# Kernel tuning notes

Measured on AMD Instinct MI355X. Metric: run time of the kernel, lower is better.

Reference implementation:

```python
import jax, jax.numpy as jnp
import numpy as np

E = 8192
K = 16
P = E * K
HIDDEN = 128
HEADS = 8
HEAD_DIM = HIDDEN // HEADS  # 16
NRAD = 64
CUTOFF = 10.0
EPS = 1e-5


def _rbf(d):
    # Gaussian radial basis expansion on [0, cutoff]
    centers = jnp.linspace(0.0, CUTOFF, NRAD)
    width = CUTOFF / NRAD
    return jnp.exp(-(((d[..., None] - centers) / width) ** 2))  # [..., NRAD]


def setup_inputs() -> dict:
    key = jax.random.key(0)
    ks = jax.random.split(key, 24)

    def lin_w(k, fi, fo):
        s = 1.0 / np.sqrt(fi)
        return jax.random.uniform(k, (fi, fo), minval=-s, maxval=s, dtype=jnp.float32)

    def lin_b(k, fi, fo):
        s = 1.0 / np.sqrt(fi)
        return jax.random.uniform(k, (fo,), minval=-s, maxval=s, dtype=jnp.float32)

    edge_features = jax.random.normal(ks[0], (E, HIDDEN), dtype=jnp.float32)
    edge_coords = jax.random.normal(ks[1], (E, 3), dtype=jnp.float32) * 3.0
    # K neighbors per edge: row index repeated, neighbor index random
    src = jnp.repeat(jnp.arange(E, dtype=jnp.int32), K)
    dst = jax.random.randint(ks[2], (P,), 0, E, dtype=jnp.int32)
    edge_pairs = jnp.stack([src, dst], axis=-1)  # [P, 2]

    mlp_in = HEAD_DIM * 2 + NRAD + 1  # 97
    return {
        "edge_features": edge_features,
        "edge_coords": edge_coords,
        "Wq": lin_w(ks[3], HIDDEN, HIDDEN),
        "Wk": lin_w(ks[4], HIDDEN, HIDDEN),
        "Wv": lin_w(ks[5], HIDDEN, HIDDEN),
        "W1": lin_w(ks[6], mlp_in, HIDDEN), "b1": lin_b(ks[7], mlp_in, HIDDEN),
        "W2": lin_w(ks[8], HIDDEN, HIDDEN), "b2": lin_b(ks[9], HIDDEN, HIDDEN),
        "W3": lin_w(ks[10], HIDDEN, HEADS), "b3": lin_b(ks[11], HIDDEN, HEADS),
        "Wg1": lin_w(ks[12], HEAD_DIM, HIDDEN), "bg1": lin_b(ks[13], HEAD_DIM, HIDDEN),
        "Wg2": lin_w(ks[14], HIDDEN, 1), "bg2": lin_b(ks[15], HIDDEN, 1),
        "Wo": lin_w(ks[16], HIDDEN, HIDDEN), "bo": lin_b(ks[17], HIDDEN, HIDDEN),
        "gamma": jnp.ones((HIDDEN,), jnp.float32),
        "beta": jnp.zeros((HIDDEN,), jnp.float32),
        "edge_pairs": edge_pairs,
    }


def reference(edge_features, edge_coords, Wq, Wk, Wv, W1, b1, W2, b2, W3, b3,
              Wg1, bg1, Wg2, bg2, Wo, bo, gamma, beta, edge_pairs):
    E_ = edge_features.shape[0]
    src = edge_pairs[:, 0]
    dst = edge_pairs[:, 1]
    silu = jax.nn.silu

    q = (edge_features @ Wq).reshape(E_, HEADS, HEAD_DIM)
    k = (edge_features @ Wk).reshape(E_, HEADS, HEAD_DIM)
    v = (edge_features @ Wv).reshape(E_, HEADS, HEAD_DIM)

    coord_diff = edge_coords[src] - edge_coords[dst]        # [P, 3]
    dist = jnp.sqrt(jnp.sum(coord_diff * coord_diff, -1))   # [P]
    rb = _rbf(dist)                                         # [P, NRAD]

    feats = []
    coords = edge_coords
    for h in range(HEADS):  # fixed small loop over structurally distinct heads
        qp = q[src, h]                                      # [P, HEAD_DIM]
        kp = k[dst, h]
        vp = v[dst, h]
        dot = jnp.sum(qp * kp, -1, keepdims=True)           # [P, 1]
        x = jnp.concatenate([qp, kp, rb, dot], axis=-1)     # [P, 97]
        hmid = silu(silu(x @ W1 + b1) @ W2 + b2)            # [P, HIDDEN]
        scores = (hmid @ W3 + b3)[:, h]                     # [P]
        # scatter softmax over destination rows (src index)
        m = jax.ops.segment_max(scores, src, num_segments=E_)
        w = jnp.exp(scores - m[src])
        denom = jax.ops.segment_sum(w, src, num_segments=E_)
        attn = w / denom[src]                               # [P]
        agg = jax.ops.segment_sum(attn[:, None] * vp, src, num_segments=E_)
        feats.append(agg)
        # equivariant coordinate update
        gate = jax.nn.sigmoid(silu(vp @ Wg1 + bg1) @ Wg2 + bg2)  # [P, 1]
        cu = jax.ops.segment_sum(attn[:, None] * gate * coord_diff, src,
                                 num_segments=E_)
        coords = coords + cu / HEADS

    uf = jnp.concatenate(feats, axis=-1)                    # [E, HIDDEN]
    y = edge_features + uf @ Wo + bo
    mean = jnp.mean(y, -1, keepdims=True)
    var = jnp.mean((y - mean) ** 2, -1, keepdims=True)
    yn = (y - mean) / jnp.sqrt(var + EPS) * gamma + beta
    return yn, coords
```

## Files before the change

kernel.cpp:

```cpp
#include <hip/hip_runtime.h>
#include <hip/hip_bf16.h>
#include <math.h>

#define E_N   8192
#define K_N   16
#define HID   128
#define HEADS 8
#define HD    16
#define NRAD  64

typedef unsigned short ushort_t;
typedef __attribute__((ext_vector_type(8))) short bf16x8;
typedef __attribute__((ext_vector_type(4))) float f32x4;
typedef __attribute__((ext_vector_type(2))) float f32x2;

__device__ __forceinline__ float fast_rcp(float x){ return __builtin_amdgcn_rcpf(x); }
__device__ __forceinline__ float silu_f(float x){ return x * fast_rcp(1.f + __expf(-x)); }
__device__ __forceinline__ float sigmoid_f(float x){ return fast_rcp(1.f + __expf(-x)); }

__device__ __forceinline__ ushort_t f2b(float x){
  union { __hip_bfloat16 b; ushort_t u; } cv;
  cv.b = __float2bfloat16(x);
  return cv.u;
}
__device__ __forceinline__ unsigned int pk_bf16(float a, float b){
  unsigned int r;
  asm volatile("v_cvt_pk_bf16_f32 %0, %1, %2" : "=v"(r) : "v"(a), "v"(b));
  return r;
}

__device__ __forceinline__ unsigned int silu2(f32x2 x){
  f32x2 t;
  t.x = __expf(-x.x);
  t.y = __expf(-x.y);
  f32x2 d = t + 1.f;
  f32x2 r;
  r.x = fast_rcp(d.x);
  r.y = fast_rcp(d.y);
  f32x2 y = x * r;
  return pk_bf16(y.x, y.y);
}

__device__ __forceinline__ void* lds_h(ushort_t* base, int row, int col){
  unsigned int byte = ((unsigned int)(row*256 + col*2)) ^ (((unsigned int)(row & 7)) << 4);
  return (void*)(reinterpret_cast<char*>(base) + byte);
}

__global__ __launch_bounds__(256) void wprep_kernel(
    const float* __restrict__ W1, const float* __restrict__ W2, const float* __restrict__ W3,
    const float* __restrict__ b1,
    const float* __restrict__ Wq, const float* __restrict__ Wk, const float* __restrict__ Wv,
    ushort_t* __restrict__ W1f, ushort_t* __restrict__ W2f, ushort_t* __restrict__ W3f,
    ushort_t* __restrict__ Wqf, ushort_t* __restrict__ Wkf, ushort_t* __restrict__ Wvf)
{
  int idx = blockIdx.x*256 + threadIdx.x;
  if (idx < 32768){
    int id  = idx & 16383;
    int i  = id & 7;
    int l  = (id >> 3) & 63;
    int nf = (id >> 9) & 7;
    int ks = (id >> 12) & 3;
    int kk = ks*32 + (l>>4)*8 + i;
    int n  = (nf>>1)*32 + 2*(l&15) + (nf&1);
    if (idx < 16384){
      float val = (kk < 97) ? W1[kk*128 + n] : (kk == 97 ? b1[n] : 0.f);
      W1f[id] = f2b(val);
    } else {
      W2f[id] = f2b(W2[kk*128 + n]);
    }
  } else if (idx < 34816){
    int id = idx - 32768;
    int i  = id & 7;
    int l  = (id >> 3) & 63;
    int ks = (id >> 9) & 3;
    int kk = ks*32 + (l>>4)*8 + i;
    int n  = l & 15;
    W3f[id] = (n < 8) ? f2b(W3[kk*8 + n]) : (ushort_t)0;
  } else if (idx < 83968){
    int id = idx - 34816;
    int m  = id >> 14;
    int r  = id & 16383;
    int i  = r & 7;
    int l  = (r >> 3) & 63;
    int nf = (r >> 9) & 7;
    int ks = (r >> 12) & 3;
    int kk = ks*32 + (l>>4)*8 + i;
    int n  = nf*16 + (l&15);
    const float* Wm = (m==0) ? Wq : ((m==1) ? Wk : Wv);
    ushort_t*    Dm = (m==0) ? Wqf : ((m==1) ? Wkf : Wvf);
    Dm[r] = f2b(Wm[kk*128 + n]);
  }
}

__global__ __launch_bounds__(256) void qkv_mfma(
    const float* __restrict__ ef,
    const ushort_t* __restrict__ Wqf, const ushort_t* __restrict__ Wkf,
    const ushort_t* __restrict__ Wvf,
    float* __restrict__ q, float* __restrict__ k, float* __restrict__ v)
{
  __shared__ __align__(16) ushort_t EfT[64*128];
  const int t = threadIdx.x;
  const int w  = t >> 6;
  const int l  = t & 63;
  const int lr = l & 15;
  const int lg = l >> 4;
  const int base = blockIdx.x * 64;

  {
    int r = t >> 2, qr = t & 3;
    const float4* src = reinterpret_cast<const float4*>(ef + (base + r)*128 + qr*32);
    #pragma unroll
    for (int i4=0;i4<8;i4++){
      float4 xv = src[i4];
      *reinterpret_cast<unsigned int*>(lds_h(EfT, r, qr*32 + i4*4    )) = pk_bf16(xv.x, xv.y);
      *reinterpret_cast<unsigned int*>(lds_h(EfT, r, qr*32 + i4*4 + 2)) = pk_bf16(xv.z, xv.w);
    }
  }
  __syncthreads();

  bf16x8 Afr[4][4];
  #pragma unroll
  for (int mf=0;mf<4;mf++)
    #pragma unroll
    for (int ks=0;ks<4;ks++)
      Afr[mf][ks] = *reinterpret_cast<const bf16x8*>(lds_h(EfT, mf*16 + lr, ks*32 + lg*8));

  #pragma unroll
  for (int m=0;m<3;m++){
    const ushort_t* Wf = (m==0) ? Wqf : ((m==1) ? Wkf : Wvf);
    float*          Om = (m==0) ? q   : ((m==1) ? k   : v);
    f32x4 acc[4][2];
    #pragma unroll
    for (int mf=0;mf<4;mf++){ acc[mf][0] = (f32x4)0.f; acc[mf][1] = (f32x4)0.f; }
    #pragma unroll
    for (int ks=0; ks<4; ks++){
      bf16x8 B0 = *reinterpret_cast<const bf16x8*>(Wf + ((ks*8 + w*2+0)*64 + l)*8);
      bf16x8 B1 = *reinterpret_cast<const bf16x8*>(Wf + ((ks*8 + w*2+1)*64 + l)*8);
      #pragma unroll
      for (int mf=0; mf<4; mf++){
        acc[mf][0] = __builtin_amdgcn_mfma_f32_16x16x32_bf16(Afr[mf][ks], B0, acc[mf][0], 0,0,0);
        acc[mf][1] = __builtin_amdgcn_mfma_f32_16x16x32_bf16(Afr[mf][ks], B1, acc[mf][1], 0,0,0);
      }
    }
    #pragma unroll
    for (int mf=0;mf<4;mf++)
      #pragma unroll
      for (int nf=0;nf<2;nf++)
        #pragma unroll
        for (int i=0;i<4;i++){
          int row = base + mf*16 + lg*4 + i;
          int col = w*32 + nf*16 + lr;
          Om[row*128 + col] = acc[mf][nf][i];
        }
  }
}

__global__ __launch_bounds__(256) void gate_kernel(
    const float* __restrict__ v,
    const float* __restrict__ Wg1, const float* __restrict__ bg1,
    const float* __restrict__ Wg2, const float* __restrict__ bg2,
    float* __restrict__ gate)
{
  const int e = blockIdx.x;
  const int t = threadIdx.x;
  const int h = t >> 5, l = t & 31;
  float vp[16];
  #pragma unroll
  for (int i=0;i<16;i++) vp[i] = v[e*128 + h*16 + i];
  float part = 0.f;
  #pragma unroll
  for (int jj=0;jj<4;jj++){
    int j = l + jj*32;
    float a = bg1[j];
    #pragma unroll
    for (int i=0;i<16;i++) a += vp[i]*Wg1[i*128+j];
    part += silu_f(a) * Wg2[j];
  }
  #pragma unroll
  for (int off=16; off>=1; off>>=1) part += __shfl_xor(part, off, 64);
  if (l==0) gate[e*8+h] = sigmoid_f(part + bg2[0]);
}

__global__ __launch_bounds__(256) void edge_attn_mfma(
    const float* __restrict__ ef, const float* __restrict__ coords,
    const float* __restrict__ q, const float* __restrict__ k, const float* __restrict__ v,
    const ushort_t* __restrict__ W1f, const ushort_t* __restrict__ W2f,
    const ushort_t* __restrict__ W3f,
    const float* __restrict__ b2, const float* __restrict__ b3,
    const float* __restrict__ Wo, const float* __restrict__ bo,
    const float* __restrict__ gamma, const float* __restrict__ beta,
    const int* __restrict__ pairs, const float* __restrict__ gate,
    float* __restrict__ out_y, float* __restrict__ out_c)
{
  __shared__ __align__(16) ushort_t BufA[128*128];
  __shared__ __align__(16) float SmallBuf[416];
  __shared__ float cd_l[16][4];
  __shared__ float gate_l[16][8];
  __shared__ int   dstl[16];

  float* sc_l   = SmallBuf;
  float* attn_l = SmallBuf + 128;
  float* feats  = SmallBuf + 256;
  float* red    = SmallBuf + 384;
  float* wopart = SmallBuf;

  const int e = blockIdx.x;
  const int t = threadIdx.x;
  const int w  = t >> 6;
  const int l  = t & 63;
  const int lr = l & 15;
  const int lg = l >> 4;

  const int pg   = lg;
  const int p    = w*4 + pg;
  const int dstp = pairs[(e*16 + p)*2 + 1];
  if (l < 4) dstl[w*4 + l] = pairs[(e*16 + w*4 + l)*2 + 1];

  float cx = coords[e*3+0]-coords[dstp*3+0];
  float cy = coords[e*3+1]-coords[dstp*3+1];
  float cz = coords[e*3+2]-coords[dstp*3+2];
  float dist = sqrtf(cx*cx+cy*cy+cz*cz);
  if (lr < 3) cd_l[p][lr] = (lr==0) ? cx : (lr==1 ? cy : cz);

  {
    int i0 = lr * 4;
    float z0 = (dist - (float)(i0+0)*(10.0f/63.0f)) * 6.4f;
    float z1 = (dist - (float)(i0+1)*(10.0f/63.0f)) * 6.4f;
    float z2 = (dist - (float)(i0+2)*(10.0f/63.0f)) * 6.4f;
    float z3 = (dist - (float)(i0+3)*(10.0f/63.0f)) * 6.4f;
    unsigned int u01 = pk_bf16(__expf(-z0*z0), __expf(-z1*z1));
    unsigned int u23 = pk_bf16(__expf(-z2*z2), __expf(-z3*z3));
    int base_row = w*32 + pg*8;
    #pragma unroll
    for (int rr=0; rr<8; rr++){
      *reinterpret_cast<unsigned int*>(lds_h(BufA, base_row+rr, 32+i0  )) = u01;
      *reinterpret_cast<unsigned int*>(lds_h(BufA, base_row+rr, 32+i0+2)) = u23;
    }
  }

  {
    const int rl  = l >> 1;
    const int hf  = l & 1;
    const int row = w*32 + rl;
    const int hh  = rl & 7;
    float dot = 0.f;
    if (hf == 0){
      const float4* qp4 = reinterpret_cast<const float4*>(q + e*128 + hh*16);
      const float4* kp4 = reinterpret_cast<const float4*>(k + dstp*128 + hh*16);
      #pragma unroll
      for (int i4=0;i4<4;i4++){
        float4 qv = qp4[i4], kv = kp4[i4];
        dot += qv.x*kv.x + qv.y*kv.y + qv.z*kv.z + qv.w*kv.w;
        *reinterpret_cast<unsigned int*>(lds_h(BufA, row, i4*4     )) = pk_bf16(qv.x, qv.y);
        *reinterpret_cast<unsigned int*>(lds_h(BufA, row, i4*4+2   )) = pk_bf16(qv.z, qv.w);
        *reinterpret_cast<unsigned int*>(lds_h(BufA, row, 16+i4*4  )) = pk_bf16(kv.x, kv.y);
        *reinterpret_cast<unsigned int*>(lds_h(BufA, row, 16+i4*4+2)) = pk_bf16(kv.z, kv.w);
      }
    }
    float dsw = __shfl_xor(dot, 1, 64);
    if (hf == 1){
      *reinterpret_cast<unsigned int*>(lds_h(BufA, row, 96)) = pk_bf16(dsw, 1.0f);
      #pragma unroll
      for (int c=98;c<128;c+=2)
        *reinterpret_cast<unsigned int*>(lds_h(BufA, row, c)) = 0u;
    }
  }
  __syncthreads();

  const int c0 = w*32 + 2*lr;
  const f32x2 b2p = { b2[c0], b2[c0+1] };

  #pragma unroll
  for (int pass=0; pass<2; ++pass){
    f32x4 acc[4][2];
    #pragma unroll
    for (int mf=0;mf<4;mf++){ acc[mf][0] = (f32x4)0.f; acc[mf][1] = (f32x4)0.f; }
    #pragma unroll
    for (int ks=0; ks<4; ks++){
      bf16x8 B0 = *reinterpret_cast<const bf16x8*>(W1f + ((ks*8 + w*2+0)*64 + l)*8);
      bf16x8 B1 = *reinterpret_cast<const bf16x8*>(W1f + ((ks*8 + w*2+1)*64 + l)*8);
      #pragma unroll
      for (int mf=0; mf<4; mf++){
        bf16x8 A = *reinterpret_cast<const bf16x8*>(lds_h(BufA, pass*64 + mf*16 + lr, ks*32 + lg*8));
        acc[mf][0] = __builtin_amdgcn_mfma_f32_16x16x32_bf16(A, B0, acc[mf][0], 0,0,0);
        acc[mf][1] = __builtin_amdgcn_mfma_f32_16x16x32_bf16(A, B1, acc[mf][1], 0,0,0);
      }
    }
    __syncthreads();
    #pragma unroll
    for (int mf=0;mf<4;mf++){
      #pragma unroll
      for (int i=0;i<4;i++){
        int row = pass*64 + mf*16 + lg*4 + i;
        f32x2 x2 = { acc[mf][0][i], acc[mf][1][i] };
        *reinterpret_cast<unsigned int*>(lds_h(BufA, row, c0)) = silu2(x2);
      }
    }
  }

  #pragma unroll
  for (int pass=0; pass<2; ++pass){
    f32x4 acc[4][2];
    #pragma unroll
    for (int mf=0;mf<4;mf++){ acc[mf][0] = (f32x4)0.f; acc[mf][1] = (f32x4)0.f; }
    #pragma unroll
    for (int ks=0; ks<4; ks++){
      bf16x8 B0 = *reinterpret_cast<const bf16x8*>(W2f + ((ks*8 + w*2+0)*64 + l)*8);
      bf16x8 B1 = *reinterpret_cast<const bf16x8*>(W2f + ((ks*8 + w*2+1)*64 + l)*8);
      #pragma unroll
      for (int mf=0; mf<4; mf++){
        bf16x8 A = *reinterpret_cast<const bf16x8*>(lds_h(BufA, pass*64 + mf*16 + lr, ks*32 + lg*8));
        acc[mf][0] = __builtin_amdgcn_mfma_f32_16x16x32_bf16(A, B0, acc[mf][0], 0,0,0);
        acc[mf][1] = __builtin_amdgcn_mfma_f32_16x16x32_bf16(A, B1, acc[mf][1], 0,0,0);
      }
    }
    __syncthreads();
    #pragma unroll
    for (int mf=0;mf<4;mf++){
      #pragma unroll
      for (int i=0;i<4;i++){
        int row = pass*64 + mf*16 + lg*4 + i;
        f32x2 x2 = (f32x2){ acc[mf][0][i], acc[mf][1][i] } + b2p;
        *reinterpret_cast<unsigned int*>(lds_h(BufA, row, c0)) = silu2(x2);
      }
    }
  }
  __syncthreads();

  {
    f32x4 a0 = (f32x4)0.f, a1 = (f32x4)0.f;
    #pragma unroll
    for (int ks=0; ks<4; ks++){
      bf16x8 B3 = *reinterpret_cast<const bf16x8*>(W3f + (ks*64 + l)*8);
      bf16x8 A0 = *reinterpret_cast<const bf16x8*>(lds_h(BufA, (w*2+0)*16 + lr, ks*32 + lg*8));
      bf16x8 A1 = *reinterpret_cast<const bf16x8*>(lds_h(BufA, (w*2+1)*16 + lr, ks*32 + lg*8));
      a0 = __builtin_amdgcn_mfma_f32_16x16x32_bf16(A0, B3, a0, 0,0,0);
      a1 = __builtin_amdgcn_mfma_f32_16x16x32_bf16(A1, B3, a1, 0,0,0);
    }
    #pragma unroll
    for (int i=0;i<4;i++){
      int rin = lg*4 + i;
      if (lr == (rin & 7)){
        sc_l[(w*2+0)*16 + rin] = a0[i] + b3[rin & 7];
        sc_l[(w*2+1)*16 + rin] = a1[i] + b3[rin & 7];
      }
    }
  }
  __syncthreads();

  if (t < 8){
    const int h = t;
    float m = -1e30f;
    for (int pp=0;pp<16;pp++) m = fmaxf(m, sc_l[pp*8+h]);
    float den = 0.f;
    for (int pp=0;pp<16;pp++){ float wgt = __expf(sc_l[pp*8+h]-m); attn_l[pp*8+h]=wgt; den += wgt; }
    float inv = fast_rcp(den);
    for (int pp=0;pp<16;pp++) attn_l[pp*8+h] *= inv;
  }
  if (t >= 128){
    int idx = t - 128; int pp = idx>>3, h = idx&7;
    gate_l[pp][h] = gate[dstl[pp]*8 + h];
  }
  __syncthreads();

  if (t < 128){
    const int h = t >> 4;
    float s = 0.f;
    #pragma unroll
    for (int pp=0;pp<16;pp++) s += attn_l[pp*8+h] * v[dstl[pp]*128 + t];
    feats[t] = s;
  }
  if (t >= 128 && t < 144){
    int pp = t-128;
    float s = 0.f;
    #pragma unroll
    for (int h=0;h<8;h++) s += attn_l[pp*8+h]*gate_l[pp][h];
    cd_l[pp][3] = s;
  }
  __syncthreads();
  if (t < 3){
    float s = 0.f;
    #pragma unroll
    for (int pp=0;pp<16;pp++) s += cd_l[pp][3]*cd_l[pp][t];
    out_c[e*3+t] = coords[e*3+t] + s*0.125f;
  }

  {
    const int col  = t & 127;
    const int half = t >> 7;
    f32x2 a2 = {0.f, 0.f};
    const float* feats2 = feats + half*64;
    const float* Wocol  = Wo + half*64*128 + col;
    #pragma unroll
    for (int iq=0; iq<32; iq++){
      f32x2 x2 = *reinterpret_cast<const f32x2*>(feats2 + iq*2);
      f32x2 w2 = { Wocol[(iq*2)*128], Wocol[(iq*2+1)*128] };
      a2 += x2 * w2;
    }
    __syncthreads();
    wopart[t] = a2.x + a2.y;
  }
  __syncthreads();

  float yv = 0.f;
  if (t < 128){
    yv = ef[e*128+t] + wopart[t] + wopart[t+128] + bo[t];
    float s1 = yv, s2 = yv*yv;
    #pragma unroll
    for (int off=32; off>=1; off>>=1){ s1 += __shfl_xor(s1,off,64); s2 += __shfl_xor(s2,off,64); }
    if ((t&63)==0){ red[(t>>6)*2+0]=s1; red[(t>>6)*2+1]=s2; }
  }
  __syncthreads();
  if (t < 128){
    float sm = red[0]+red[2], sq = red[1]+red[3];
    float mean = sm * (1.f/128.f);
    float var  = sq * (1.f/128.f) - mean*mean;
    float rstd = rsqrtf(var + 1e-5f);
    out_y[e*128+t] = (yv-mean)*rstd*gamma[t] + beta[t];
  }
}

extern "C" void kernel_launch(void* const* d_in, const int* in_sizes, int n_in,
                              void* d_out, int out_size, void* d_ws, size_t ws_size,
                              hipStream_t stream)
{
  const float* ef     = (const float*)d_in[0];
  const float* coords = (const float*)d_in[1];
  const float* Wq  = (const float*)d_in[2];
  const float* Wk  = (const float*)d_in[3];
  const float* Wv  = (const float*)d_in[4];
  const float* W1  = (const float*)d_in[5];
  const float* b1  = (const float*)d_in[6];
  const float* W2  = (const float*)d_in[7];
  const float* b2  = (const float*)d_in[8];
  const float* W3  = (const float*)d_in[9];
  const float* b3  = (const float*)d_in[10];
  const float* Wg1 = (const float*)d_in[11];
  const float* bg1 = (const float*)d_in[12];
  const float* Wg2 = (const float*)d_in[13];
  const float* bg2 = (const float*)d_in[14];
  const float* Wo  = (const float*)d_in[15];
  const float* bo  = (const float*)d_in[16];
  const float* gamma = (const float*)d_in[17];
  const float* beta  = (const float*)d_in[18];
  const int*   pairs = (const int*)d_in[19];

  float* ws   = (float*)d_ws;
  float* q    = ws;
  float* k    = q + E_N*HID;
  float* v    = k + E_N*HID;
  float* gate = v + E_N*HID;
  ushort_t* W1f = (ushort_t*)(gate + E_N*HEADS);
  ushort_t* W2f = W1f + 16384;
  ushort_t* W3f = W2f + 16384;
  ushort_t* Wqf = W3f + 2048;
  ushort_t* Wkf = Wqf + 16384;
  ushort_t* Wvf = Wkf + 16384;

  wprep_kernel<<<328, 256, 0, stream>>>(W1, W2, W3, b1, Wq, Wk, Wv,
      W1f, W2f, W3f, Wqf, Wkf, Wvf);
  qkv_mfma<<<E_N/64, 256, 0, stream>>>(ef, Wqf, Wkf, Wvf, q, k, v);
  gate_kernel<<<E_N, 256, 0, stream>>>(v, Wg1, bg1, Wg2, bg2, gate);
  edge_attn_mfma<<<E_N, 256, 0, stream>>>(ef, coords, q, k, v,
      W1f, W2f, W3f, b2, b3, Wo, bo, gamma, beta, pairs, gate,
      (float*)d_out, (float*)d_out + E_N*HID);
}
```

Baseline: 195.3 us.

## Split edge MLP rows across eight waves instead of two-pass loop

Launches the edge attention kernel with 512 threads so the 128-row MLP tile is split across eight waves (two row halves by four column slices), removing the two-pass loop per layer. The score projection now uses one 16-row tile per wave. Setup, Wo projection and reductions are limited to the first 256 threads. This raises per-block parallelism but leaves half the threads idle in several stages, adds barriers, and may reduce the number of resident blocks per CU.

```diff
diff --git a/kernel.cpp b/kernel.cpp
--- a/kernel.cpp
+++ b/kernel.cpp
@@ -181,7 +181,7 @@
   if (l==0) gate[e*8+h] = sigmoid_f(part + bg2[0]);
 }
 
-__global__ __launch_bounds__(256) void edge_attn_mfma(
+__global__ __launch_bounds__(512) void edge_attn_mfma(
     const float* __restrict__ ef, const float* __restrict__ coords,
     const float* __restrict__ q, const float* __restrict__ k, const float* __restrict__ v,
     const ushort_t* __restrict__ W1f, const ushort_t* __restrict__ W2f,
@@ -211,139 +211,134 @@
   const int lr = l & 15;
   const int lg = l >> 4;
 
-  const int pg   = lg;
-  const int p    = w*4 + pg;
-  const int dstp = pairs[(e*16 + p)*2 + 1];
-  if (l < 4) dstl[w*4 + l] = pairs[(e*16 + w*4 + l)*2 + 1];
-
-  float cx = coords[e*3+0]-coords[dstp*3+0];
-  float cy = coords[e*3+1]-coords[dstp*3+1];
-  float cz = coords[e*3+2]-coords[dstp*3+2];
-  float dist = sqrtf(cx*cx+cy*cy+cz*cz);
-  if (lr < 3) cd_l[p][lr] = (lr==0) ? cx : (lr==1 ? cy : cz);
+  if (t < 256){
+    const int pg   = lg;
+    const int p    = w*4 + pg;
+    const int dstp = pairs[(e*16 + p)*2 + 1];
+    if (l < 4) dstl[w*4 + l] = pairs[(e*16 + w*4 + l)*2 + 1];
+
+    float cx = coords[e*3+0]-coords[dstp*3+0];
+    float cy = coords[e*3+1]-coords[dstp*3+1];
+    float cz = coords[e*3+2]-coords[dstp*3+2];
+    float dist = sqrtf(cx*cx+cy*cy+cz*cz);
+    if (lr < 3) cd_l[p][lr] = (lr==0) ? cx : (lr==1 ? cy : cz);
+
+    {
+      int i0 = lr * 4;
+      float z0 = (dist - (float)(i0+0)*(10.0f/63.0f)) * 6.4f;
+      float z1 = (dist - (float)(i0+1)*(10.0f/63.0f)) * 6.4f;
+      float z2 = (dist - (float)(i0+2)*(10.0f/63.0f)) * 6.4f;
+      float z3 = (dist - (float)(i0+3)*(10.0f/63.0f)) * 6.4f;
+      unsigned int u01 = pk_bf16(__expf(-z0*z0), __expf(-z1*z1));
+      unsigned int u23 = pk_bf16(__expf(-z2*z2), __expf(-z3*z3));
+      int base_row = w*32 + pg*8;
+      #pragma unroll
+      for (int rr=0; rr<8; rr++){
+        *reinterpret_cast<unsigned int*>(lds_h(BufA, base_row+rr, 32+i0  )) = u01;
+        *reinterpret_cast<unsigned int*>(lds_h(BufA, base_row+rr, 32+i0+2)) = u23;
+      }
+    }
+
+    {
+      const int rl  = l >> 1;
+      const int hf  = l & 1;
+      const int row = w*32 + rl;
+      const int hh  = rl & 7;
+      float dot = 0.f;
+      if (hf == 0){
+        const float4* qp4 = reinterpret_cast<const float4*>(q + e*128 + hh*16);
+        const float4* kp4 = reinterpret_cast<const float4*>(k + dstp*128 + hh*16);
+        #pragma unroll
+        for (int i4=0;i4<4;i4++){
+          float4 qv = qp4[i4], kv = kp4[i4];
+          dot += qv.x*kv.x + qv.y*kv.y + qv.z*kv.z + qv.w*kv.w;
+          *reinterpret_cast<unsigned int*>(lds_h(BufA, row, i4*4     )) = pk_bf16(qv.x, qv.y);
+          *reinterpret_cast<unsigned int*>(lds_h(BufA, row, i4*4+2   )) = pk_bf16(qv.z, qv.w);
+          *reinterpret_cast<unsigned int*>(lds_h(BufA, row, 16+i4*4  )) = pk_bf16(kv.x, kv.y);
+          *reinterpret_cast<unsigned int*>(lds_h(BufA, row, 16+i4*4+2)) = pk_bf16(kv.z, kv.w);
+        }
+      }
+      float dsw = __shfl_xor(dot, 1, 64);
+      if (hf == 1){
+        *reinterpret_cast<unsigned int*>(lds_h(BufA, row, 96)) = pk_bf16(dsw, 1.0f);
+        #pragma unroll
+        for (int c=98;c<128;c+=2)
+          *reinterpret_cast<unsigned int*>(lds_h(BufA, row, c)) = 0u;
+      }
+    }
+  }
+  __syncthreads();
+
+  const int wm = w >> 2;
+  const int wn = w & 3;
+  const int c0 = wn*32 + 2*lr;
+  const f32x2 b2p = { b2[c0], b2[c0+1] };
+
+  f32x4 acc[4][2];
+
+  #pragma unroll
+  for (int mf=0;mf<4;mf++){ acc[mf][0] = (f32x4)0.f; acc[mf][1] = (f32x4)0.f; }
+  #pragma unroll
+  for (int ks=0; ks<4; ks++){
+    bf16x8 B0 = *reinterpret_cast<const bf16x8*>(W1f + ((ks*8 + wn*2+0)*64 + l)*8);
+    bf16x8 B1 = *reinterpret_cast<const bf16x8*>(W1f + ((ks*8 + wn*2+1)*64 + l)*8);
+    #pragma unroll
+    for (int mf=0; mf<4; mf++){
+      bf16x8 A = *reinterpret_cast<const bf16x8*>(lds_h(BufA, wm*64 + mf*16 + lr, ks*32 + lg*8));
+      acc[mf][0] = __builtin_amdgcn_mfma_f32_16x16x32_bf16(A, B0, acc[mf][0], 0,0,0);
+      acc[mf][1] = __builtin_amdgcn_mfma_f32_16x16x32_bf16(A, B1, acc[mf][1], 0,0,0);
+    }
+  }
+  __syncthreads();
+  #pragma unroll
+  for (int mf=0;mf<4;mf++){
+    #pragma unroll
+    for (int i=0;i<4;i++){
+      int row = wm*64 + mf*16 + lg*4 + i;
+      f32x2 x2 = { acc[mf][0][i], acc[mf][1][i] };
+      *reinterpret_cast<unsigned int*>(lds_h(BufA, row, c0)) = silu2(x2);
+    }
+  }
+  __syncthreads();
+
+  #pragma unroll
+  for (int mf=0;mf<4;mf++){ acc[mf][0] = (f32x4)0.f; acc[mf][1] = (f32x4)0.f; }
+  #pragma unroll
+  for (int ks=0; ks<4; ks++){
+    bf16x8 B0 = *reinterpret_cast<const bf16x8*>(W2f + ((ks*8 + wn*2+0)*64 + l)*8);
+    bf16x8 B1 = *reinterpret_cast<const bf16x8*>(W2f + ((ks*8 + wn*2+1)*64 + l)*8);
+    #pragma unroll
+    for (int mf=0; mf<4; mf++){
+      bf16x8 A = *reinterpret_cast<const bf16x8*>(lds_h(BufA, wm*64 + mf*16 + lr, ks*32 + lg*8));
+      acc[mf][0] = __builtin_amdgcn_mfma_f32_16x16x32_bf16(A, B0, acc[mf][0], 0,0,0);
+      acc[mf][1] = __builtin_amdgcn_mfma_f32_16x16x32_bf16(A, B1, acc[mf][1], 0,0,0);
+    }
+  }
+  __syncthreads();
+  #pragma unroll
+  for (int mf=0;mf<4;mf++){
+    #pragma unroll
+    for (int i=0;i<4;i++){
+      int row = wm*64 + mf*16 + lg*4 + i;
+      f32x2 x2 = (f32x2){ acc[mf][0][i], acc[mf][1][i] } + b2p;
+      *reinterpret_cast<unsigned int*>(lds_h(BufA, row, c0)) = silu2(x2);
+    }
+  }
+  __syncthreads();
 
   {
-    int i0 = lr * 4;
-    float z0 = (dist - (float)(i0+0)*(10.0f/63.0f)) * 6.4f;
-    float z1 = (dist - (float)(i0+1)*(10.0f/63.0f)) * 6.4f;
-    float z2 = (dist - (float)(i0+2)*(10.0f/63.0f)) * 6.4f;
-    float z3 = (dist - (float)(i0+3)*(10.0f/63.0f)) * 6.4f;
-    unsigned int u01 = pk_bf16(__expf(-z0*z0), __expf(-z1*z1));
-    unsigned int u23 = pk_bf16(__expf(-z2*z2), __expf(-z3*z3));
-    int base_row = w*32 + pg*8;
-    #pragma unroll
-    for (int rr=0; rr<8; rr++){
-      *reinterpret_cast<unsigned int*>(lds_h(BufA, base_row+rr, 32+i0  )) = u01;
-      *reinterpret_cast<unsigned int*>(lds_h(BufA, base_row+rr, 32+i0+2)) = u23;
-    }
-  }
-
-  {
-    const int rl  = l >> 1;
-    const int hf  = l & 1;
-    const int row = w*32 + rl;
-    const int hh  = rl & 7;
-    float dot = 0.f;
-    if (hf == 0){
-      const float4* qp4 = reinterpret_cast<const float4*>(q + e*128 + hh*16);
-      const float4* kp4 = reinterpret_cast<const float4*>(k + dstp*128 + hh*16);
-      #pragma unroll
-      for (int i4=0;i4<4;i4++){
-        float4 qv = qp4[i4], kv = kp4[i4];
-        dot += qv.x*kv.x + qv.y*kv.y + qv.z*kv.z + qv.w*kv.w;
-        *reinterpret_cast<unsigned int*>(lds_h(BufA, row, i4*4     )) = pk_bf16(qv.x, qv.y);
-        *reinterpret_cast<unsigned int*>(lds_h(BufA, row, i4*4+2   )) = pk_bf16(qv.z, qv.w);
-        *reinterpret_cast<unsigned int*>(lds_h(BufA, row, 16+i4*4  )) = pk_bf16(kv.x, kv.y);
-        *reinterpret_cast<unsigned int*>(lds_h(BufA, row, 16+i4*4+2)) = pk_bf16(kv.z, kv.w);
-      }
-    }
-    float dsw = __shfl_xor(dot, 1, 64);
-    if (hf == 1){
-      *reinterpret_cast<unsigned int*>(lds_h(BufA, row, 96)) = pk_bf16(dsw, 1.0f);
-      #pragma unroll
-      for (int c=98;c<128;c+=2)
-        *reinterpret_cast<unsigned int*>(lds_h(BufA, row, c)) = 0u;
-    }
-  }
-  __syncthreads();
-
-  const int c0 = w*32 + 2*lr;
-  const f32x2 b2p = { b2[c0], b2[c0+1] };
-
-  #pragma unroll
-  for (int pass=0; pass<2; ++pass){
-    f32x4 acc[4][2];
-    #pragma unroll
-    for (int mf=0;mf<4;mf++){ acc[mf][0] = (f32x4)0.f; acc[mf][1] = (f32x4)0.f; }
-    #pragma unroll
-    for (int ks=0; ks<4; ks++){
-      bf16x8 B0 = *reinterpret_cast<const bf16x8*>(W1f + ((ks*8 + w*2+0)*64 + l)*8);
-      bf16x8 B1 = *reinterpret_cast<const bf16x8*>(W1f + ((ks*8 + w*2+1)*64 + l)*8);
-      #pragma unroll
-      for (int mf=0; mf<4; mf++){
-        bf16x8 A = *reinterpret_cast<const bf16x8*>(lds_h(BufA, pass*64 + mf*16 + lr, ks*32 + lg*8));
-        acc[mf][0] = __builtin_amdgcn_mfma_f32_16x16x32_bf16(A, B0, acc[mf][0], 0,0,0);
-        acc[mf][1] = __builtin_amdgcn_mfma_f32_16x16x32_bf16(A, B1, acc[mf][1], 0,0,0);
-      }
-    }
-    __syncthreads();
-    #pragma unroll
-    for (int mf=0;mf<4;mf++){
-      #pragma unroll
-      for (int i=0;i<4;i++){
-        int row = pass*64 + mf*16 + lg*4 + i;
-        f32x2 x2 = { acc[mf][0][i], acc[mf][1][i] };
-        *reinterpret_cast<unsigned int*>(lds_h(BufA, row, c0)) = silu2(x2);
-      }
-    }
-  }
-
-  #pragma unroll
-  for (int pass=0; pass<2; ++pass){
-    f32x4 acc[4][2];
-    #pragma unroll
-    for (int mf=0;mf<4;mf++){ acc[mf][0] = (f32x4)0.f; acc[mf][1] = (f32x4)0.f; }
-    #pragma unroll
-    for (int ks=0; ks<4; ks++){
-      bf16x8 B0 = *reinterpret_cast<const bf16x8*>(W2f + ((ks*8 + w*2+0)*64 + l)*8);
-      bf16x8 B1 = *reinterpret_cast<const bf16x8*>(W2f + ((ks*8 + w*2+1)*64 + l)*8);
-      #pragma unroll
-      for (int mf=0; mf<4; mf++){
-        bf16x8 A = *reinterpret_cast<const bf16x8*>(lds_h(BufA, pass*64 + mf*16 + lr, ks*32 + lg*8));
-        acc[mf][0] = __builtin_amdgcn_mfma_f32_16x16x32_bf16(A, B0, acc[mf][0], 0,0,0);
-        acc[mf][1] = __builtin_amdgcn_mfma_f32_16x16x32_bf16(A, B1, acc[mf][1], 0,0,0);
-      }
-    }
-    __syncthreads();
-    #pragma unroll
-    for (int mf=0;mf<4;mf++){
-      #pragma unroll
-      for (int i=0;i<4;i++){
-        int row = pass*64 + mf*16 + lg*4 + i;
-        f32x2 x2 = (f32x2){ acc[mf][0][i], acc[mf][1][i] } + b2p;
-        *reinterpret_cast<unsigned int*>(lds_h(BufA, row, c0)) = silu2(x2);
-      }
-    }
-  }
-  __syncthreads();
-
-  {
-    f32x4 a0 = (f32x4)0.f, a1 = (f32x4)0.f;
+    f32x4 a0 = (f32x4)0.f;
     #pragma unroll
     for (int ks=0; ks<4; ks++){
       bf16x8 B3 = *reinterpret_cast<const bf16x8*>(W3f + (ks*64 + l)*8);
-      bf16x8 A0 = *reinterpret_cast<const bf16x8*>(lds_h(BufA, (w*2+0)*16 + lr, ks*32 + lg*8));
-      bf16x8 A1 = *reinterpret_cast<const bf16x8*>(lds_h(BufA, (w*2+1)*16 + lr, ks*32 + lg*8));
+      bf16x8 A0 = *reinterpret_cast<const bf16x8*>(lds_h(BufA, w*16 + lr, ks*32 + lg*8));
       a0 = __builtin_amdgcn_mfma_f32_16x16x32_bf16(A0, B3, a0, 0,0,0);
-      a1 = __builtin_amdgcn_mfma_f32_16x16x32_bf16(A1, B3, a1, 0,0,0);
     }
     #pragma unroll
     for (int i=0;i<4;i++){
       int rin = lg*4 + i;
-      if (lr == (rin & 7)){
-        sc_l[(w*2+0)*16 + rin] = a0[i] + b3[rin & 7];
-        sc_l[(w*2+1)*16 + rin] = a1[i] + b3[rin & 7];
-      }
+      if (lr == (rin & 7))
+        sc_l[w*16 + rin] = a0[i] + b3[rin & 7];
     }
   }
   __syncthreads();
@@ -357,7 +352,7 @@
     float inv = fast_rcp(den);
     for (int pp=0;pp<16;pp++) attn_l[pp*8+h] *= inv;
   }
-  if (t >= 128){
+  if (t >= 128 && t < 256){
     int idx = t - 128; int pp = idx>>3, h = idx&7;
     gate_l[pp][h] = gate[dstl[pp]*8 + h];
   }
@@ -385,10 +380,10 @@
     out_c[e*3+t] = coords[e*3+t] + s*0.125f;
   }
 
-  {
+  f32x2 a2 = {0.f, 0.f};
+  if (t < 256){
     const int col  = t & 127;
     const int half = t >> 7;
-    f32x2 a2 = {0.f, 0.f};
     const float* feats2 = feats + half*64;
     const float* Wocol  = Wo + half*64*128 + col;
     #pragma unroll
@@ -397,9 +392,9 @@
       f32x2 w2 = { Wocol[(iq*2)*128], Wocol[(iq*2+1)*128] };
       a2 += x2 * w2;
     }
-    __syncthreads();
-    wopart[t] = a2.x + a2.y;
-  }
+  }
+  __syncthreads();
+  if (t < 256) wopart[t] = a2.x + a2.y;
   __syncthreads();
 
   float yv = 0.f;
@@ -461,7 +456,7 @@
       W1f, W2f, W3f, Wqf, Wkf, Wvf);
   qkv_mfma<<<E_N/64, 256, 0, stream>>>(ef, Wqf, Wkf, Wvf, q, k, v);
   gate_kernel<<<E_N, 256, 0, stream>>>(v, Wg1, bg1, Wg2, bg2, gate);
-  edge_attn_mfma<<<E_N, 256, 0, stream>>>(ef, coords, q, k, v,
+  edge_attn_mfma<<<E_N, 512, 0, stream>>>(ef, coords, q, k, v,
       W1f, W2f, W3f, b2, b3, Wo, bo, gamma, beta, pairs, gate,
       (float*)d_out, (float*)d_out + E_N*HID);
 }
```

Result: slower. 216.0 us (+10.6%).

## Chain edge MLP layers in registers via transposed MFMA instead of LDS round-trips

Applied to the files above, without the earlier changes.

The three-layer edge MLP now runs in transposed form: each wave keeps its 32 rows of input in registers, computes W1^T·X with the weight as the A operand, and feeds the SiLU-packed bf16 accumulators directly as B operands to 16x16x16 MFMAs for W2 and W3. This removes the intermediate LDS writes, reads and __syncthreads between layers, and the weight prep kernel emits new transposed fragment layouts to match. In exchange it holds more live registers, which could lower occupancy, and it uses the smaller-K MFMA shape for the second and third layers.

```diff
diff --git a/kernel.cpp b/kernel.cpp
--- a/kernel.cpp
+++ b/kernel.cpp
@@ -11,6 +11,7 @@
 
 typedef unsigned short ushort_t;
 typedef __attribute__((ext_vector_type(8))) short bf16x8;
+typedef __attribute__((ext_vector_type(4))) short bf16x4;
 typedef __attribute__((ext_vector_type(4))) float f32x4;
 typedef __attribute__((ext_vector_type(2))) float f32x2;
 
@@ -40,6 +41,21 @@
   f32x2 y = x * r;
   return pk_bf16(y.x, y.y);
 }
+__device__ __forceinline__ bf16x4 silu_pack4(f32x4 x){
+  union { unsigned int u[2]; bf16x4 v; } cv;
+  cv.u[0] = silu2((f32x2){x[0], x[1]});
+  cv.u[1] = silu2((f32x2){x[2], x[3]});
+  return cv.v;
+}
+
+__device__ __forceinline__ f32x4 mfma16(bf16x4 a, bf16x4 b, f32x4 c){
+#if __has_builtin(__builtin_amdgcn_mfma_f32_16x16x16bf16_1k)
+  return __builtin_amdgcn_mfma_f32_16x16x16bf16_1k(a, b, c, 0, 0, 0);
+#else
+  asm volatile("v_mfma_f32_16x16x16_bf16 %0, %1, %2, %0" : "+v"(c) : "v"(a), "v"(b));
+  return c;
+#endif
+}
 
 __device__ __forceinline__ void* lds_h(ushort_t* base, int row, int col){
   unsigned int byte = ((unsigned int)(row*256 + col*2)) ^ (((unsigned int)(row & 7)) << 4);
@@ -50,32 +66,36 @@
     const float* __restrict__ W1, const float* __restrict__ W2, const float* __restrict__ W3,
     const float* __restrict__ b1,
     const float* __restrict__ Wq, const float* __restrict__ Wk, const float* __restrict__ Wv,
-    ushort_t* __restrict__ W1f, ushort_t* __restrict__ W2f, ushort_t* __restrict__ W3f,
+    ushort_t* __restrict__ W1t, ushort_t* __restrict__ W2t, ushort_t* __restrict__ W3t,
     ushort_t* __restrict__ Wqf, ushort_t* __restrict__ Wkf, ushort_t* __restrict__ Wvf)
 {
   int idx = blockIdx.x*256 + threadIdx.x;
-  if (idx < 32768){
-    int id  = idx & 16383;
-    int i  = id & 7;
-    int l  = (id >> 3) & 63;
-    int nf = (id >> 9) & 7;
-    int ks = (id >> 12) & 3;
+  if (idx < 16384){
+    int i  = idx & 7;
+    int l  = (idx >> 3) & 63;
+    int ks = (idx >> 9) & 3;
+    int ff = (idx >> 11) & 7;
     int kk = ks*32 + (l>>4)*8 + i;
-    int n  = (nf>>1)*32 + 2*(l&15) + (nf&1);
-    if (idx < 16384){
-      float val = (kk < 97) ? W1[kk*128 + n] : (kk == 97 ? b1[n] : 0.f);
-      W1f[id] = f2b(val);
-    } else {
-      W2f[id] = f2b(W2[kk*128 + n]);
-    }
+    int f  = ff*16 + (l&15);
+    float val = (kk < 97) ? W1[kk*128 + f] : (kk == 97 ? b1[f] : 0.f);
+    W1t[idx] = f2b(val);
+  } else if (idx < 32768){
+    int id = idx - 16384;
+    int i  = id & 3;
+    int l  = (id >> 2) & 63;
+    int ks = (id >> 8) & 7;
+    int gf = (id >> 11) & 7;
+    int f  = ks*16 + (l>>4)*4 + i;
+    int g  = gf*16 + (l&15);
+    W2t[id] = f2b(W2[f*128 + g]);
   } else if (idx < 34816){
     int id = idx - 32768;
-    int i  = id & 7;
-    int l  = (id >> 3) & 63;
-    int ks = (id >> 9) & 3;
-    int kk = ks*32 + (l>>4)*8 + i;
+    int i  = id & 3;
+    int l  = (id >> 2) & 63;
+    int ks = (id >> 8) & 7;
+    int g  = ks*16 + (l>>4)*4 + i;
     int n  = l & 15;
-    W3f[id] = (n < 8) ? f2b(W3[kk*8 + n]) : (ushort_t)0;
+    W3t[id] = (n < 8) ? f2b(W3[g*8 + n]) : (ushort_t)0;
   } else if (idx < 83968){
     int id = idx - 34816;
     int m  = id >> 14;
@@ -184,8 +204,8 @@
 __global__ __launch_bounds__(256) void edge_attn_mfma(
     const float* __restrict__ ef, const float* __restrict__ coords,
     const float* __restrict__ q, const float* __restrict__ k, const float* __restrict__ v,
-    const ushort_t* __restrict__ W1f, const ushort_t* __restrict__ W2f,
-    const ushort_t* __restrict__ W3f,
+    const ushort_t* __restrict__ W1t, const ushort_t* __restrict__ W2t,
+    const ushort_t* __restrict__ W3t,
     const float* __restrict__ b2, const float* __restrict__ b3,
     const float* __restrict__ Wo, const float* __restrict__ bo,
     const float* __restrict__ gamma, const float* __restrict__ beta,
@@ -267,84 +287,53 @@
   }
   __syncthreads();
 
-  const int c0 = w*32 + 2*lr;
-  const f32x2 b2p = { b2[c0], b2[c0+1] };
-
-  #pragma unroll
-  for (int pass=0; pass<2; ++pass){
-    f32x4 acc[4][2];
-    #pragma unroll
-    for (int mf=0;mf<4;mf++){ acc[mf][0] = (f32x4)0.f; acc[mf][1] = (f32x4)0.f; }
+  bf16x8 Xb[2][4];
+  #pragma unroll
+  for (int rf=0; rf<2; rf++)
+    #pragma unroll
+    for (int ks=0; ks<4; ks++)
+      Xb[rf][ks] = *reinterpret_cast<const bf16x8*>(
+          lds_h(BufA, w*32 + rf*16 + lr, ks*32 + lg*8));
+
+  bf16x4 B1s[8][2];
+  #pragma unroll
+  for (int ff=0; ff<8; ff++){
+    f32x4 a0 = (f32x4)0.f, a1 = (f32x4)0.f;
     #pragma unroll
     for (int ks=0; ks<4; ks++){
-      bf16x8 B0 = *reinterpret_cast<const bf16x8*>(W1f + ((ks*8 + w*2+0)*64 + l)*8);
-      bf16x8 B1 = *reinterpret_cast<const bf16x8*>(W1f + ((ks*8 + w*2+1)*64 + l)*8);
-      #pragma unroll
-      for (int mf=0; mf<4; mf++){
-        bf16x8 A = *reinterpret_cast<const bf16x8*>(lds_h(BufA, pass*64 + mf*16 + lr, ks*32 + lg*8));
-        acc[mf][0] = __builtin_amdgcn_mfma_f32_16x16x32_bf16(A, B0, acc[mf][0], 0,0,0);
-        acc[mf][1] = __builtin_amdgcn_mfma_f32_16x16x32_bf16(A, B1, acc[mf][1], 0,0,0);
-      }
-    }
-    __syncthreads();
-    #pragma unroll
-    for (int mf=0;mf<4;mf++){
-      #pragma unroll
-      for (int i=0;i<4;i++){
-        int row = pass*64 + mf*16 + lg*4 + i;
-        f32x2 x2 = { acc[mf][0][i], acc[mf][1][i] };
-        *reinterpret_cast<unsigned int*>(lds_h(BufA, row, c0)) = silu2(x2);
-      }
-    }
-  }
-
-  #pragma unroll
-  for (int pass=0; pass<2; ++pass){
-    f32x4 acc[4][2];
-    #pragma unroll
-    for (int mf=0;mf<4;mf++){ acc[mf][0] = (f32x4)0.f; acc[mf][1] = (f32x4)0.f; }
-    #pragma unroll
-    for (int ks=0; ks<4; ks++){
-      bf16x8 B0 = *reinterpret_cast<const bf16x8*>(W2f + ((ks*8 + w*2+0)*64 + l)*8);
-      bf16x8 B1 = *reinterpret_cast<const bf16x8*>(W2f + ((ks*8 + w*2+1)*64 + l)*8);
-      #pragma unroll
-      for (int mf=0; mf<4; mf++){
-        bf16x8 A = *reinterpret_cast<const bf16x8*>(lds_h(BufA, pass*64 + mf*16 + lr, ks*32 + lg*8));
-        acc[mf][0] = __builtin_amdgcn_mfma_f32_16x16x32_bf16(A, B0, acc[mf][0], 0,0,0);
-        acc[mf][1] = __builtin_amdgcn_mfma_f32_16x16x32_bf16(A, B1, acc[mf][1], 0,0,0);
-      }
-    }
-    __syncthreads();
-    #pragma unroll
-    for (int mf=0;mf<4;mf++){
-      #pragma unroll
-      for (int i=0;i<4;i++){
-        int row = pass*64 + mf*16 + lg*4 + i;
-        f32x2 x2 = (f32x2){ acc[mf][0][i], acc[mf][1][i] } + b2p;
-        *reinterpret_cast<unsigned int*>(lds_h(BufA, row, c0)) = silu2(x2);
-      }
-    }
-  }
-  __syncthreads();
-
-  {
-    f32x4 a0 = (f32x4)0.f, a1 = (f32x4)0.f;
-    #pragma unroll
-    for (int ks=0; ks<4; ks++){
-      bf16x8 B3 = *reinterpret_cast<const bf16x8*>(W3f + (ks*64 + l)*8);
-      bf16x8 A0 = *reinterpret_cast<const bf16x8*>(lds_h(BufA, (w*2+0)*16 + lr, ks*32 + lg*8));
-      bf16x8 A1 = *reinterpret_cast<const bf16x8*>(lds_h(BufA, (w*2+1)*16 + lr, ks*32 + lg*8));
-      a0 = __builtin_amdgcn_mfma_f32_16x16x32_bf16(A0, B3, a0, 0,0,0);
-      a1 = __builtin_amdgcn_mfma_f32_16x16x32_bf16(A1, B3, a1, 0,0,0);
-    }
-    #pragma unroll
-    for (int i=0;i<4;i++){
-      int rin = lg*4 + i;
-      if (lr == (rin & 7)){
-        sc_l[(w*2+0)*16 + rin] = a0[i] + b3[rin & 7];
-        sc_l[(w*2+1)*16 + rin] = a1[i] + b3[rin & 7];
-      }
-    }
+      bf16x8 A = *reinterpret_cast<const bf16x8*>(W1t + (ff*2048 + ks*512 + l*8));
+      a0 = __builtin_amdgcn_mfma_f32_16x16x32_bf16(A, Xb[0][ks], a0, 0,0,0);
+      a1 = __builtin_amdgcn_mfma_f32_16x16x32_bf16(A, Xb[1][ks], a1, 0,0,0);
+    }
+    B1s[ff][0] = silu_pack4(a0);
+    B1s[ff][1] = silu_pack4(a1);
+  }
+
+  f32x4 s0 = (f32x4)0.f, s1 = (f32x4)0.f;
+  #pragma unroll
+  for (int gf=0; gf<8; gf++){
+    f32x4 c0 = (f32x4)0.f, c1 = (f32x4)0.f;
+    #pragma unroll
+    for (int ks=0; ks<8; ks++){
+      bf16x4 A2 = *reinterpret_cast<const bf16x4*>(W2t + (gf*2048 + ks*256 + l*4));
+      c0 = mfma16(A2, B1s[ks][0], c0);
+      c1 = mfma16(A2, B1s[ks][1], c1);
+    }
+    f32x4 b2v = *reinterpret_cast<const f32x4*>(b2 + gf*16 + lg*4);
+    c0 += b2v;
+    c1 += b2v;
+    bf16x4 h0 = silu_pack4(c0);
+    bf16x4 h1 = silu_pack4(c1);
+    bf16x4 A3 = *reinterpret_cast<const bf16x4*>(W3t + (gf*256 + l*4));
+    s0 = mfma16(A3, h0, s0);
+    s1 = mfma16(A3, h1, s1);
+  }
+
+  if (lg == ((l & 7) >> 2)){
+    int i = l & 3;
+    float b3v = b3[l & 7];
+    sc_l[w*32 +      lr] = s0[i] + b3v;
+    sc_l[w*32 + 16 + lr] = s1[i] + b3v;
   }
   __syncthreads();
 
@@ -405,10 +394,10 @@
   float yv = 0.f;
   if (t < 128){
     yv = ef[e*128+t] + wopart[t] + wopart[t+128] + bo[t];
-    float s1 = yv, s2 = yv*yv;
-    #pragma unroll
-    for (int off=32; off>=1; off>>=1){ s1 += __shfl_xor(s1,off,64); s2 += __shfl_xor(s2,off,64); }
-    if ((t&63)==0){ red[(t>>6)*2+0]=s1; red[(t>>6)*2+1]=s2; }
+    float s1v = yv, s2v = yv*yv;
+    #pragma unroll
+    for (int off=32; off>=1; off>>=1){ s1v += __shfl_xor(s1v,off,64); s2v += __shfl_xor(s2v,off,64); }
+    if ((t&63)==0){ red[(t>>6)*2+0]=s1v; red[(t>>6)*2+1]=s2v; }
   }
   __syncthreads();
   if (t < 128){
@@ -450,18 +439,18 @@
   float* k    = q + E_N*HID;
   float* v    = k + E_N*HID;
   float* gate = v + E_N*HID;
-  ushort_t* W1f = (ushort_t*)(gate + E_N*HEADS);
-  ushort_t* W2f = W1f + 16384;
-  ushort_t* W3f = W2f + 16384;
-  ushort_t* Wqf = W3f + 2048;
+  ushort_t* W1t = (ushort_t*)(gate + E_N*HEADS);
+  ushort_t* W2t = W1t + 16384;
+  ushort_t* W3t = W2t + 16384;
+  ushort_t* Wqf = W3t + 2048;
   ushort_t* Wkf = Wqf + 16384;
   ushort_t* Wvf = Wkf + 16384;
 
   wprep_kernel<<<328, 256, 0, stream>>>(W1, W2, W3, b1, Wq, Wk, Wv,
-      W1f, W2f, W3f, Wqf, Wkf, Wvf);
+      W1t, W2t, W3t, Wqf, Wkf, Wvf);
   qkv_mfma<<<E_N/64, 256, 0, stream>>>(ef, Wqf, Wkf, Wvf, q, k, v);
   gate_kernel<<<E_N, 256, 0, stream>>>(v, Wg1, bg1, Wg2, bg2, gate);
   edge_attn_mfma<<<E_N, 256, 0, stream>>>(ef, coords, q, k, v,
-      W1f, W2f, W3f, b2, b3, Wo, bo, gamma, beta, pairs, gate,
+      W1t, W2t, W3t, b2, b3, Wo, bo, gamma, beta, pairs, gate,
       (float*)d_out, (float*)d_out + E_N*HID);
 }
```

Result: slower. 209.5 us (+7.3%).
